# Kernel tuning notes

Hardware: AMD Instinct MI355X
Metric: run time of the kernel (lower is better)

Reference implementation:

```python
import jax, jax.numpy as jnp
import numpy as np

B, C, H, W = 8, 128, 48, 48
GROUPS = 32
EPS = 1e-5


def group_norm(x, w, b):
    # x: [B,C,H,W] -> normalize within 32 groups over (C//G, H, W)
    xg = x.reshape(B, GROUPS, C // GROUPS, H, W)
    mu = xg.mean(axis=(2, 3, 4), keepdims=True)
    var = xg.var(axis=(2, 3, 4), keepdims=True)
    xg = (xg - mu) * jax.lax.rsqrt(var + EPS)
    return xg.reshape(B, C, H, W) * w[None, :, None, None] + b[None, :, None, None]


def conv1x1(x, w, b):
    # pointwise conv: [B,C,H,W], w: [Cout,Cin], b: [Cout]
    return jnp.einsum('oc,bchw->bohw', w, x) + b[None, :, None, None]


def setup_inputs() -> dict:
    key = jax.random.key(0)
    ks = jax.random.split(key, 6)
    s = 1.0 / np.sqrt(C)
    return {
        'x': jax.random.normal(ks[0], (B, C, H, W), jnp.float32),
        'gn_w': jnp.ones((C,), jnp.float32),
        'gn_b': jnp.zeros((C,), jnp.float32),
        'wq': jax.random.normal(ks[1], (C, C), jnp.float32) * s,
        'bq': jnp.zeros((C,), jnp.float32),
        'wk': jax.random.normal(ks[2], (C, C), jnp.float32) * s,
        'bk': jnp.zeros((C,), jnp.float32),
        'wv': jax.random.normal(ks[3], (C, C), jnp.float32) * s,
        'bv': jnp.zeros((C,), jnp.float32),
        'wo': jax.random.normal(ks[4], (C, C), jnp.float32) * s,
        'bo': jnp.zeros((C,), jnp.float32),
    }


def reference(x, gn_w, gn_b, wq, bq, wk, bk, wv, bv, wo, bo):
    xn = group_norm(x, gn_w, gn_b)
    q = conv1x1(xn, wq, bq)
    k = conv1x1(xn, wk, bk)
    v = conv1x1(xn, wv, bv)
    # scores: [B,H,W,I,J]
    scores = jnp.einsum('bchw,bcij->bhwij', q, k) / jnp.sqrt(jnp.float32(C))
    # NOTE: original calls F.softmax with no dim; torch picks dim=1 (the query-H axis)
    attn = jax.nn.softmax(scores, axis=1)
    ctx = jnp.einsum('bhwnm,bcnm->bchw', attn, v)
    return x + conv1x1(ctx, wo, bo)
```

## Files before the change

kernel.cpp:

```cpp
#include <hip/hip_runtime.h>
#include <hip/hip_bf16.h>

typedef short s16x8 __attribute__((ext_vector_type(8)));
typedef float f32x4 __attribute__((ext_vector_type(4)));
typedef int   i32x4 __attribute__((ext_vector_type(4)));
typedef unsigned short u16;

#define BB 8
#define CC 128
#define HH 48
#define WW 48
#define NN 2304
#define SCALE_L2E 0.12751744f
#define SZ_MAP (BB*CC*NN)
#define NSPLIT 3
#define TILES_PER (18/NSPLIT)

__device__ inline u16 f2bf(float f) {
    unsigned u = __builtin_bit_cast(unsigned, f);
    u = (u + 0x7FFFu + ((u >> 16) & 1u)) >> 16;
    return (u16)u;
}
__device__ inline float bf2f(u16 h) {
    unsigned u = ((unsigned)h) << 16;
    return __builtin_bit_cast(float, u);
}

#define MFMA(a, b, c) __builtin_amdgcn_mfma_f32_16x16x32_bf16(a, b, c, 0, 0, 0)
#define DPP_ROR_ADD(x, N) { \
    int yi_ = __builtin_amdgcn_update_dpp(0, __builtin_bit_cast(int, x), 0x120 | (N), 0xf, 0xf, true); \
    x += __builtin_bit_cast(float, yi_); }

__global__ __launch_bounds__(256) void gnprep_kernel(
        const float* __restrict__ x, const float* __restrict__ gw,
        const float* __restrict__ gb, u16* __restrict__ xnT,
        const float* __restrict__ wq, const float* __restrict__ wk,
        const float* __restrict__ wv_, const float* __restrict__ wo,
        u16* __restrict__ w16) {
    int tid = threadIdx.x;
    if (blockIdx.x >= 256) {
        int i = (blockIdx.x - 256) * 256 + tid;
        int m = i >> 14, r = i & 16383;
        const float* src = (m == 0) ? wq : (m == 1) ? wk : (m == 2) ? wv_ : wo;
        w16[i] = f2bf(src[r]);
        return;
    }
    int b = blockIdx.x & 7, g = blockIdx.x >> 3;
    const float* xb = x + ((size_t)b * CC + g * 4) * NN;
    float v[4][9];
    float s = 0.f, ss = 0.f;
#pragma unroll
    for (int c = 0; c < 4; ++c)
#pragma unroll
        for (int k = 0; k < 9; ++k) {
            float t = xb[c * NN + tid + k * 256];
            v[c][k] = t; s += t; ss += t * t;
        }
#pragma unroll
    for (int o = 32; o > 0; o >>= 1) { s += __shfl_down(s, o); ss += __shfl_down(ss, o); }
    __shared__ float red[8];
    __shared__ float stats[2];
    int wid = tid >> 6;
    if ((tid & 63) == 0) { red[wid * 2] = s; red[wid * 2 + 1] = ss; }
    __syncthreads();
    if (tid == 0) {
        float S = 0.f, SS = 0.f;
        for (int i = 0; i < 4; ++i) { S += red[i * 2]; SS += red[i * 2 + 1]; }
        float mu = S * (1.f / 9216.f);
        float var = SS * (1.f / 9216.f) - mu * mu;
        stats[0] = mu;
        stats[1] = rsqrtf(var + 1e-5f);
    }
    __syncthreads();
    float mu = stats[0], rs = stats[1];
    float sc[4], bi[4];
#pragma unroll
    for (int c = 0; c < 4; ++c) {
        sc[c] = gw[g * 4 + c] * rs;
        bi[c] = gb[g * 4 + c] - mu * sc[c];
    }
#pragma unroll
    for (int k = 0; k < 9; ++k) {
        int n = tid + k * 256;
        ushort4 o;
        o.x = f2bf(v[0][k] * sc[0] + bi[0]);
        o.y = f2bf(v[1][k] * sc[1] + bi[1]);
        o.z = f2bf(v[2][k] * sc[2] + bi[2]);
        o.w = f2bf(v[3][k] * sc[3] + bi[3]);
        *(ushort4*)(xnT + ((size_t)b * NN + n) * CC + g * 4) = o;
    }
}

__global__ __launch_bounds__(256) void qkv_kernel(
        const u16* __restrict__ xnT, const u16* __restrict__ w16,
        const float* __restrict__ bq, const float* __restrict__ bk,
        const float* __restrict__ bv,
        u16* __restrict__ qT, u16* __restrict__ kt2, u16* __restrict__ vt2) {
    int b = blockIdx.x, n0 = blockIdx.y * 128, z = blockIdx.z;
    int tid = threadIdx.x, lane = tid & 63, wvw = tid >> 6;
    int l15 = lane & 15, l4 = lane >> 4;
    const u16* xb = xnT + (size_t)b * NN * CC;

    if (z == 0) {
        const u16* w16q = w16;
        const u16* w16k = w16 + 16384;
        u16* kb = kt2 + (size_t)b * NN * CC;
        s16x8 xa[2][4];
#pragma unroll
        for (int mf = 0; mf < 2; ++mf)
#pragma unroll
            for (int ks = 0; ks < 4; ++ks)
                xa[mf][ks] = *(const s16x8*)(xb + (size_t)(n0 + wvw * 32 + mf * 16 + l15) * CC + ks * 32 + l4 * 8);
        int chunk = blockIdx.y * 4 + wvw;
#pragma unroll 2
        for (int nf = 0; nf < 8; ++nf) {
            f32x4 aq[2] = {}, ak[2] = {};
#pragma unroll
            for (int ks = 0; ks < 4; ++ks) {
                s16x8 fq = *(const s16x8*)(w16q + (nf * 16 + l15) * CC + ks * 32 + l4 * 8);
                s16x8 fk = *(const s16x8*)(w16k + (nf * 16 + l15) * CC + ks * 32 + l4 * 8);
#pragma unroll
                for (int mf = 0; mf < 2; ++mf) {
                    aq[mf] = MFMA(fq, xa[mf][ks], aq[mf]);
                    ak[mf] = MFMA(fk, xa[mf][ks], ak[mf]);
                }
            }
            int cob = nf * 16 + l4 * 4;
            float4 bq4 = *(const float4*)(bq + cob);
            float4 bk4 = *(const float4*)(bk + cob);
#pragma unroll
            for (int mf = 0; mf < 2; ++mf) {
                int n = n0 + wvw * 32 + mf * 16 + l15;
                ushort4 qo;
                qo.x = f2bf((aq[mf][0] + bq4.x) * SCALE_L2E);
                qo.y = f2bf((aq[mf][1] + bq4.y) * SCALE_L2E);
                qo.z = f2bf((aq[mf][2] + bq4.z) * SCALE_L2E);
                qo.w = f2bf((aq[mf][3] + bq4.w) * SCALE_L2E);
                *(ushort4*)(qT + ((size_t)b * NN + n) * CC + cob) = qo;
                int n5 = mf * 16 + l15;
                int slot = ((n5 & 4) << 2) + ((n5 & 24) >> 1) + (n5 & 3);
                ushort4 ko;
                ko.x = f2bf(ak[mf][0] + bk4.x);
                ko.y = f2bf(ak[mf][1] + bk4.y);
                ko.z = f2bf(ak[mf][2] + bk4.z);
                ko.w = f2bf(ak[mf][3] + bk4.w);
                *(ushort4*)(kb + (size_t)chunk * 4096 + (cob >> 5) * 1024 + slot * 32 + (cob & 31)) = ko;
            }
        }
    } else {
        const u16* w16v = w16 + 2 * 16384;
        u16* vb = vt2 + (size_t)b * NN * CC;
        s16x8 wa[2][4];
#pragma unroll
        for (int mf = 0; mf < 2; ++mf)
#pragma unroll
            for (int ks = 0; ks < 4; ++ks)
                wa[mf][ks] = *(const s16x8*)(w16v + (wvw * 32 + mf * 16 + l15) * CC + ks * 32 + l4 * 8);
        float bvl[2];
        bvl[0] = bv[wvw * 32 + l15];
        bvl[1] = bv[wvw * 32 + 16 + l15];
#pragma unroll 2
        for (int nf = 0; nf < 8; ++nf) {
            f32x4 av[2] = {};
#pragma unroll
            for (int ks = 0; ks < 4; ++ks) {
                s16x8 xf = *(const s16x8*)(xb + (size_t)(n0 + nf * 16 + l15) * CC + ks * 32 + l4 * 8);
#pragma unroll
                for (int mf = 0; mf < 2; ++mf) av[mf] = MFMA(xf, wa[mf][ks], av[mf]);
            }
            int chunk = blockIdx.y * 4 + (nf >> 1);
            int nlo = (nf & 1) * 16 + l4 * 4;
#pragma unroll
            for (int mf = 0; mf < 2; ++mf) {
                ushort4 vo;
                vo.x = f2bf(av[mf][0] + bvl[mf]);
                vo.y = f2bf(av[mf][1] + bvl[mf]);
                vo.z = f2bf(av[mf][2] + bvl[mf]);
                vo.w = f2bf(av[mf][3] + bvl[mf]);
                *(ushort4*)(vb + (size_t)chunk * 4096 + (wvw * 2 + mf) * 512 + l15 * 32 + nlo) = vo;
            }
        }
    }
}

#define TILE_BODY(T, KFC, KFN) { \
    const u16* cv = vb + (size_t)((T) * 4 + wvw) * 4096; \
    s16x8 vf[8]; \
    _Pragma("unroll") \
    for (int cf = 0; cf < 8; ++cf) \
        vf[cf] = *(const s16x8*)(cv + cf * 512 + l15 * 32 + l4 * 8); \
    f32x4 sf[2][3] = {}; \
    __builtin_amdgcn_s_setprio(1); \
    _Pragma("unroll") \
    for (int ks = 0; ks < 4; ++ks) \
        _Pragma("unroll") \
        for (int mf = 0; mf < 2; ++mf) \
            _Pragma("unroll") \
            for (int hf = 0; hf < 3; ++hf) \
                sf[mf][hf] = MFMA(KFC[mf][ks], qf[hf][ks], sf[mf][hf]); \
    __builtin_amdgcn_s_setprio(0); \
    { \
        int tn_ = ((T) + 1 < 18) ? (T) + 1 : 0; \
        const u16* cbn_ = kb + (size_t)(tn_ * 4 + wvw) * 4096; \
        _Pragma("unroll") \
        for (int mf = 0; mf < 2; ++mf) \
            _Pragma("unroll") \
            for (int ks = 0; ks < 4; ++ks) \
                KFN[mf][ks] = *(const s16x8*)(cbn_ + ks * 1024 + (mf * 16 + l15) * 32 + l4 * 8); \
    } \
    float p[2][3][4]; \
    _Pragma("unroll") \
    for (int mf = 0; mf < 2; ++mf) \
        _Pragma("unroll") \
        for (int hf = 0; hf < 3; ++hf) \
            _Pragma("unroll") \
            for (int r = 0; r < 4; ++r) p[mf][hf][r] = __builtin_amdgcn_exp2f(sf[mf][hf][r]); \
    float den[2][4]; \
    _Pragma("unroll") \
    for (int mf = 0; mf < 2; ++mf) \
        _Pragma("unroll") \
        for (int r = 0; r < 4; ++r) \
            den[mf][r] = p[mf][0][r] + p[mf][1][r] + p[mf][2][r]; \
    _Pragma("unroll") \
    for (int mf = 0; mf < 2; ++mf) \
        _Pragma("unroll") \
        for (int r = 0; r < 4; ++r) { \
            DPP_ROR_ADD(den[mf][r], 1); \
            DPP_ROR_ADD(den[mf][r], 2); \
            DPP_ROR_ADD(den[mf][r], 4); \
            DPP_ROR_ADD(den[mf][r], 8); \
        } \
    float rd[2][4]; \
    _Pragma("unroll") \
    for (int mf = 0; mf < 2; ++mf) \
        _Pragma("unroll") \
        for (int r = 0; r < 4; ++r) rd[mf][r] = __builtin_amdgcn_rcpf(den[mf][r]); \
    s16x8 pbf[3]; \
    _Pragma("unroll") \
    for (int hf = 0; hf < 3; ++hf) { \
        unsigned u0, u1, u2, u3; \
        float a0 = p[0][hf][0] * rd[0][0], a1 = p[0][hf][1] * rd[0][1]; \
        float a2 = p[0][hf][2] * rd[0][2], a3 = p[0][hf][3] * rd[0][3]; \
        float a4 = p[1][hf][0] * rd[1][0], a5 = p[1][hf][1] * rd[1][1]; \
        float a6 = p[1][hf][2] * rd[1][2], a7 = p[1][hf][3] * rd[1][3]; \
        asm("v_cvt_pk_bf16_f32 %0, %1, %2" : "=v"(u0) : "v"(a0), "v"(a1)); \
        asm("v_cvt_pk_bf16_f32 %0, %1, %2" : "=v"(u1) : "v"(a2), "v"(a3)); \
        asm("v_cvt_pk_bf16_f32 %0, %1, %2" : "=v"(u2) : "v"(a4), "v"(a5)); \
        asm("v_cvt_pk_bf16_f32 %0, %1, %2" : "=v"(u3) : "v"(a6), "v"(a7)); \
        i32x4 bb2 = { (int)u0, (int)u1, (int)u2, (int)u3 }; \
        pbf[hf] = __builtin_bit_cast(s16x8, bb2); \
    } \
    __builtin_amdgcn_s_setprio(1); \
    _Pragma("unroll") \
    for (int cf = 0; cf < 8; ++cf) \
        _Pragma("unroll") \
        for (int hf = 0; hf < 3; ++hf) \
            cacc[cf][hf] = MFMA(vf[cf], pbf[hf], cacc[cf][hf]); \
    __builtin_amdgcn_s_setprio(0); \
}

__global__ __launch_bounds__(256, 2) void attn_kernel(
        const u16* __restrict__ qT, const u16* __restrict__ kt2,
        const u16* __restrict__ vt2, u16* __restrict__ part) {
    int b = blockIdx.x, w = blockIdx.y, sp = blockIdx.z;
    int tid = threadIdx.x, lane = tid & 63, wvw = tid >> 6;
    int l15 = lane & 15, l4 = lane >> 4;
    __shared__ float red[4 * 48 * 36];

    const u16* qb = qT + (size_t)b * NN * CC;
    const u16* kb = kt2 + (size_t)b * NN * CC;
    const u16* vb = vt2 + (size_t)b * NN * CC;

    s16x8 qf[3][4];
#pragma unroll
    for (int hf = 0; hf < 3; ++hf)
#pragma unroll
        for (int ks = 0; ks < 4; ++ks)
            qf[hf][ks] = *(const s16x8*)(qb + (size_t)((hf * 16 + l15) * WW + w) * CC + ks * 32 + l4 * 8);

    f32x4 cacc[8][3] = {};

    const int tbase = sp * TILES_PER;

    s16x8 kfA[2][4], kfB[2][4];
    {
        const u16* cb = kb + (size_t)(tbase * 4 + wvw) * 4096;
#pragma unroll
        for (int mf = 0; mf < 2; ++mf)
#pragma unroll
            for (int ks = 0; ks < 4; ++ks)
                kfA[mf][ks] = *(const s16x8*)(cb + ks * 1024 + (mf * 16 + l15) * 32 + l4 * 8);
    }

#pragma unroll 1
    for (int tt = 0; tt < TILES_PER; tt += 2) {
        int t0 = tbase + tt;
        TILE_BODY(t0, kfA, kfB)
        int t1 = tbase + tt + 1;
        TILE_BODY(t1, kfB, kfA)
    }

#pragma unroll
    for (int s = 0; s < 4; ++s) {
        if (s) __syncthreads();
#pragma unroll
        for (int q = 0; q < 4; ++q) {
            if (((q - wvw) & 3) == s) {
#pragma unroll
                for (int i = 0; i < 2; ++i) {
                    int cf = 2 * q + i;
#pragma unroll
                    for (int hf = 0; hf < 3; ++hf) {
                        int addr = q * 1728 + (hf * 16 + l15) * 36 + i * 16 + 4 * l4;
                        f32x4* pp = (f32x4*)&red[addr];
                        if (s == 0) *pp = cacc[cf][hf];
                        else { f32x4 tv = *pp; tv += cacc[cf][hf]; *pp = tv; }
                    }
                }
            }
        }
    }
    __syncthreads();
    u16* po = part + (size_t)(b * NSPLIT + sp) * NN * CC;
#pragma unroll
    for (int pass = 0; pass < 12; ++pass) {
        int h = pass * 4 + l4;
        int c = wvw * 32 + l15 * 2;
        float2 v2 = *(float2*)&red[wvw * 1728 + h * 36 + l15 * 2];
        unsigned pk;
        asm("v_cvt_pk_bf16_f32 %0, %1, %2" : "=v"(pk) : "v"(v2.x), "v"(v2.y));
        *(unsigned*)(po + (size_t)(h * WW + w) * CC + c) = pk;
    }
}

__global__ __launch_bounds__(256) void out_kernel(
        const u16* __restrict__ part, const u16* __restrict__ w16o,
        const float* __restrict__ bo, const float* __restrict__ x,
        float* __restrict__ out) {
    int b = blockIdx.x, n0 = blockIdx.y * 128;
    int tid = threadIdx.x, lane = tid & 63, wvw = tid >> 6;
    int l15 = lane & 15, l4 = lane >> 4;
    const u16* pb = part + (size_t)b * NSPLIT * NN * CC;
    s16x8 bfr[2][4];
#pragma unroll
    for (int nf = 0; nf < 2; ++nf)
#pragma unroll
        for (int ks = 0; ks < 4; ++ks) {
            size_t off = (size_t)(n0 + wvw * 32 + nf * 16 + l15) * CC + ks * 32 + l4 * 8;
            s16x8 v0 = *(const s16x8*)(pb + off);
            s16x8 v1 = *(const s16x8*)(pb + (size_t)NN * CC + off);
            s16x8 v2 = *(const s16x8*)(pb + (size_t)2 * NN * CC + off);
            s16x8 o;
#pragma unroll
            for (int j = 0; j < 8; ++j)
                o[j] = (short)f2bf(bf2f((u16)v0[j]) + bf2f((u16)v1[j]) + bf2f((u16)v2[j]));
            bfr[nf][ks] = o;
        }
#pragma unroll 2
    for (int mf = 0; mf < 8; ++mf) {
        s16x8 af[4];
#pragma unroll
        for (int ks = 0; ks < 4; ++ks)
            af[ks] = *(const s16x8*)(w16o + (mf * 16 + l15) * CC + ks * 32 + l4 * 8);
        f32x4 acc[2] = {};
#pragma unroll
        for (int ks = 0; ks < 4; ++ks)
#pragma unroll
            for (int nf = 0; nf < 2; ++nf)
                acc[nf] = MFMA(af[ks], bfr[nf][ks], acc[nf]);
#pragma unroll
        for (int nf = 0; nf < 2; ++nf)
#pragma unroll
            for (int r = 0; r < 4; ++r) {
                int co = mf * 16 + l4 * 4 + r;
                int n = n0 + wvw * 32 + nf * 16 + l15;
                size_t idx = ((size_t)b * CC + co) * NN + n;
                out[idx] = acc[nf][r] + bo[co] + x[idx];
            }
    }
}

extern "C" void kernel_launch(void* const* d_in, const int* in_sizes, int n_in,
                              void* d_out, int out_size, void* d_ws, size_t ws_size,
                              hipStream_t stream) {
    const float* x  = (const float*)d_in[0];
    const float* gw = (const float*)d_in[1];
    const float* gb = (const float*)d_in[2];
    const float* wq = (const float*)d_in[3];
    const float* bq = (const float*)d_in[4];
    const float* wk = (const float*)d_in[5];
    const float* bk = (const float*)d_in[6];
    const float* wv_ = (const float*)d_in[7];
    const float* bv = (const float*)d_in[8];
    const float* wo = (const float*)d_in[9];
    const float* bo = (const float*)d_in[10];

    u16* ws   = (u16*)d_ws;
    u16* xnT  = ws;
    u16* qT   = ws + (size_t)SZ_MAP;
    u16* kt2  = ws + (size_t)2 * SZ_MAP;
    u16* vt2  = ws + (size_t)3 * SZ_MAP;
    u16* part = ws + (size_t)4 * SZ_MAP;
    u16* w16  = ws + (size_t)(4 + NSPLIT) * SZ_MAP;
    float* out = (float*)d_out;

    gnprep_kernel<<<512, 256, 0, stream>>>(x, gw, gb, xnT, wq, wk, wv_, wo, w16);
    qkv_kernel<<<dim3(8, 18, 2), 256, 0, stream>>>(xnT, w16, bq, bk, bv, qT, kt2, vt2);
    attn_kernel<<<dim3(8, WW, NSPLIT), 256, 0, stream>>>(qT, kt2, vt2, part);
    out_kernel<<<dim3(8, 18), 256, 0, stream>>>(part, w16 + 3 * 16384, bo, x, out);
}
```

Baseline: 84.78 us.

## Restructure attention to share K/V chunks via LDS across eight w-waves

The attention kernel now assigns one w-column per wave (eight waves per 512-thread block). K/V chunks are staged into double-buffered LDS with global_load_lds and shared by all waves, which removes the old cross-wave LDS reduction. The goal is less redundant global K/V traffic. NSPLIT rises to 4. The QKV kernel splits Q and K into separate z-slices for more parallelism, and the output kernel splits output channels across two z-blocks and writes float4-vectorized output. The cost is a __syncthreads per chunk, an extra partial buffer to read and sum, and a higher register load from holding full cacc per wave.

New measurement: 77.59 us. 8.5% less time.

```diff
diff --git a/kernel.cpp b/kernel.cpp
--- a/kernel.cpp
+++ b/kernel.cpp
@@ -13,8 +13,8 @@
 #define NN 2304
 #define SCALE_L2E 0.12751744f
 #define SZ_MAP (BB*CC*NN)
-#define NSPLIT 3
-#define TILES_PER (18/NSPLIT)
+#define NSPLIT 4
+#define CHPER (72/NSPLIT)
 
 __device__ inline u16 f2bf(float f) {
     unsigned u = __builtin_bit_cast(unsigned, f);
@@ -103,31 +103,24 @@
 
     if (z == 0) {
         const u16* w16q = w16;
-        const u16* w16k = w16 + 16384;
-        u16* kb = kt2 + (size_t)b * NN * CC;
         s16x8 xa[2][4];
 #pragma unroll
         for (int mf = 0; mf < 2; ++mf)
 #pragma unroll
             for (int ks = 0; ks < 4; ++ks)
                 xa[mf][ks] = *(const s16x8*)(xb + (size_t)(n0 + wvw * 32 + mf * 16 + l15) * CC + ks * 32 + l4 * 8);
-        int chunk = blockIdx.y * 4 + wvw;
 #pragma unroll 2
         for (int nf = 0; nf < 8; ++nf) {
-            f32x4 aq[2] = {}, ak[2] = {};
+            f32x4 aq[2] = {};
 #pragma unroll
             for (int ks = 0; ks < 4; ++ks) {
                 s16x8 fq = *(const s16x8*)(w16q + (nf * 16 + l15) * CC + ks * 32 + l4 * 8);
-                s16x8 fk = *(const s16x8*)(w16k + (nf * 16 + l15) * CC + ks * 32 + l4 * 8);
-#pragma unroll
-                for (int mf = 0; mf < 2; ++mf) {
+#pragma unroll
+                for (int mf = 0; mf < 2; ++mf)
                     aq[mf] = MFMA(fq, xa[mf][ks], aq[mf]);
-                    ak[mf] = MFMA(fk, xa[mf][ks], ak[mf]);
-                }
             }
             int cob = nf * 16 + l4 * 4;
             float4 bq4 = *(const float4*)(bq + cob);
-            float4 bk4 = *(const float4*)(bk + cob);
 #pragma unroll
             for (int mf = 0; mf < 2; ++mf) {
                 int n = n0 + wvw * 32 + mf * 16 + l15;
@@ -137,6 +130,32 @@
                 qo.z = f2bf((aq[mf][2] + bq4.z) * SCALE_L2E);
                 qo.w = f2bf((aq[mf][3] + bq4.w) * SCALE_L2E);
                 *(ushort4*)(qT + ((size_t)b * NN + n) * CC + cob) = qo;
+            }
+        }
+    } else if (z == 1) {
+        const u16* w16k = w16 + 16384;
+        u16* kb = kt2 + (size_t)b * NN * CC;
+        s16x8 xa[2][4];
+#pragma unroll
+        for (int mf = 0; mf < 2; ++mf)
+#pragma unroll
+            for (int ks = 0; ks < 4; ++ks)
+                xa[mf][ks] = *(const s16x8*)(xb + (size_t)(n0 + wvw * 32 + mf * 16 + l15) * CC + ks * 32 + l4 * 8);
+        int chunk = blockIdx.y * 4 + wvw;
+#pragma unroll 2
+        for (int nf = 0; nf < 8; ++nf) {
+            f32x4 ak[2] = {};
+#pragma unroll
+            for (int ks = 0; ks < 4; ++ks) {
+                s16x8 fk = *(const s16x8*)(w16k + (nf * 16 + l15) * CC + ks * 32 + l4 * 8);
+#pragma unroll
+                for (int mf = 0; mf < 2; ++mf)
+                    ak[mf] = MFMA(fk, xa[mf][ks], ak[mf]);
+            }
+            int cob = nf * 16 + l4 * 4;
+            float4 bk4 = *(const float4*)(bk + cob);
+#pragma unroll
+            for (int mf = 0; mf < 2; ++mf) {
                 int n5 = mf * 16 + l15;
                 int slot = ((n5 & 4) << 2) + ((n5 & 24) >> 1) + (n5 & 3);
                 ushort4 ko;
@@ -183,44 +202,43 @@
     }
 }
 
-#define TILE_BODY(T, KFC, KFN) { \
-    const u16* cv = vb + (size_t)((T) * 4 + wvw) * 4096; \
-    s16x8 vf[8]; \
-    _Pragma("unroll") \
-    for (int cf = 0; cf < 8; ++cf) \
-        vf[cf] = *(const s16x8*)(cv + cf * 512 + l15 * 32 + l4 * 8); \
+#define STAGE(CH, KD, VD) { \
+    const u16* ks_ = kb + (size_t)(CH) * 4096 + wvw * 512 + lane * 8; \
+    const u16* vs_ = vb + (size_t)(CH) * 4096 + wvw * 512 + lane * 8; \
+    __builtin_amdgcn_global_load_lds((const __attribute__((address_space(1))) void*)ks_, \
+        (__attribute__((address_space(3))) void*)(KD + wvw * 512), 16, 0, 0); \
+    __builtin_amdgcn_global_load_lds((const __attribute__((address_space(1))) void*)vs_, \
+        (__attribute__((address_space(3))) void*)(VD + wvw * 512), 16, 0, 0); \
+}
+
+#define CHUNK_BODY(CH, KC, VC, KN, VN) { \
+    { int nx_ = ((CH) + 1 < 72) ? (CH) + 1 : 0; STAGE(nx_, KN, VN) } \
     f32x4 sf[2][3] = {}; \
     __builtin_amdgcn_s_setprio(1); \
     _Pragma("unroll") \
-    for (int ks = 0; ks < 4; ++ks) \
-        _Pragma("unroll") \
-        for (int mf = 0; mf < 2; ++mf) \
-            _Pragma("unroll") \
-            for (int hf = 0; hf < 3; ++hf) \
-                sf[mf][hf] = MFMA(KFC[mf][ks], qf[hf][ks], sf[mf][hf]); \
+    for (int ks = 0; ks < 4; ++ks) { \
+        s16x8 kf0 = *(const s16x8*)(KC + ks * 1024 + l15 * 32 + l4 * 8); \
+        s16x8 kf1 = *(const s16x8*)(KC + ks * 1024 + (16 + l15) * 32 + l4 * 8); \
+        _Pragma("unroll") \
+        for (int hf = 0; hf < 3; ++hf) { \
+            sf[0][hf] = MFMA(kf0, qf[hf][ks], sf[0][hf]); \
+            sf[1][hf] = MFMA(kf1, qf[hf][ks], sf[1][hf]); \
+        } \
+    } \
     __builtin_amdgcn_s_setprio(0); \
-    { \
-        int tn_ = ((T) + 1 < 18) ? (T) + 1 : 0; \
-        const u16* cbn_ = kb + (size_t)(tn_ * 4 + wvw) * 4096; \
-        _Pragma("unroll") \
-        for (int mf = 0; mf < 2; ++mf) \
-            _Pragma("unroll") \
-            for (int ks = 0; ks < 4; ++ks) \
-                KFN[mf][ks] = *(const s16x8*)(cbn_ + ks * 1024 + (mf * 16 + l15) * 32 + l4 * 8); \
-    } \
-    float p[2][3][4]; \
+    float pe[2][3][4]; \
     _Pragma("unroll") \
     for (int mf = 0; mf < 2; ++mf) \
         _Pragma("unroll") \
         for (int hf = 0; hf < 3; ++hf) \
             _Pragma("unroll") \
-            for (int r = 0; r < 4; ++r) p[mf][hf][r] = __builtin_amdgcn_exp2f(sf[mf][hf][r]); \
+            for (int r = 0; r < 4; ++r) pe[mf][hf][r] = __builtin_amdgcn_exp2f(sf[mf][hf][r]); \
     float den[2][4]; \
     _Pragma("unroll") \
     for (int mf = 0; mf < 2; ++mf) \
         _Pragma("unroll") \
         for (int r = 0; r < 4; ++r) \
-            den[mf][r] = p[mf][0][r] + p[mf][1][r] + p[mf][2][r]; \
+            den[mf][r] = pe[mf][0][r] + pe[mf][1][r] + pe[mf][2][r]; \
     _Pragma("unroll") \
     for (int mf = 0; mf < 2; ++mf) \
         _Pragma("unroll") \
@@ -239,10 +257,10 @@
     _Pragma("unroll") \
     for (int hf = 0; hf < 3; ++hf) { \
         unsigned u0, u1, u2, u3; \
-        float a0 = p[0][hf][0] * rd[0][0], a1 = p[0][hf][1] * rd[0][1]; \
-        float a2 = p[0][hf][2] * rd[0][2], a3 = p[0][hf][3] * rd[0][3]; \
-        float a4 = p[1][hf][0] * rd[1][0], a5 = p[1][hf][1] * rd[1][1]; \
-        float a6 = p[1][hf][2] * rd[1][2], a7 = p[1][hf][3] * rd[1][3]; \
+        float a0 = pe[0][hf][0] * rd[0][0], a1 = pe[0][hf][1] * rd[0][1]; \
+        float a2 = pe[0][hf][2] * rd[0][2], a3 = pe[0][hf][3] * rd[0][3]; \
+        float a4 = pe[1][hf][0] * rd[1][0], a5 = pe[1][hf][1] * rd[1][1]; \
+        float a6 = pe[1][hf][2] * rd[1][2], a7 = pe[1][hf][3] * rd[1][3]; \
         asm("v_cvt_pk_bf16_f32 %0, %1, %2" : "=v"(u0) : "v"(a0), "v"(a1)); \
         asm("v_cvt_pk_bf16_f32 %0, %1, %2" : "=v"(u1) : "v"(a2), "v"(a3)); \
         asm("v_cvt_pk_bf16_f32 %0, %1, %2" : "=v"(u2) : "v"(a4), "v"(a5)); \
@@ -252,20 +270,24 @@
     } \
     __builtin_amdgcn_s_setprio(1); \
     _Pragma("unroll") \
-    for (int cf = 0; cf < 8; ++cf) \
+    for (int cf = 0; cf < 8; ++cf) { \
+        s16x8 vf = *(const s16x8*)(VC + cf * 512 + l15 * 32 + l4 * 8); \
         _Pragma("unroll") \
         for (int hf = 0; hf < 3; ++hf) \
-            cacc[cf][hf] = MFMA(vf[cf], pbf[hf], cacc[cf][hf]); \
+            cacc[cf][hf] = MFMA(vf, pbf[hf], cacc[cf][hf]); \
+    } \
     __builtin_amdgcn_s_setprio(0); \
-}
-
-__global__ __launch_bounds__(256, 2) void attn_kernel(
+    __syncthreads(); \
+}
+
+__global__ __launch_bounds__(512, 2) void attn_kernel(
         const u16* __restrict__ qT, const u16* __restrict__ kt2,
         const u16* __restrict__ vt2, u16* __restrict__ part) {
-    int b = blockIdx.x, w = blockIdx.y, sp = blockIdx.z;
+    int b = blockIdx.x, sp = blockIdx.z;
     int tid = threadIdx.x, lane = tid & 63, wvw = tid >> 6;
+    int w = blockIdx.y * 8 + wvw;
     int l15 = lane & 15, l4 = lane >> 4;
-    __shared__ float red[4 * 48 * 36];
+    __shared__ u16 kbA[4096], vbA[4096], kbB[4096], vbB[4096];
 
     const u16* qb = qT + (size_t)b * NN * CC;
     const u16* kb = kt2 + (size_t)b * NN * CC;
@@ -280,64 +302,38 @@
 
     f32x4 cacc[8][3] = {};
 
-    const int tbase = sp * TILES_PER;
-
-    s16x8 kfA[2][4], kfB[2][4];
-    {
-        const u16* cb = kb + (size_t)(tbase * 4 + wvw) * 4096;
-#pragma unroll
-        for (int mf = 0; mf < 2; ++mf)
-#pragma unroll
-            for (int ks = 0; ks < 4; ++ks)
-                kfA[mf][ks] = *(const s16x8*)(cb + ks * 1024 + (mf * 16 + l15) * 32 + l4 * 8);
-    }
+    const int cbase = sp * CHPER;
+    STAGE(cbase, kbA, vbA)
+    __syncthreads();
 
 #pragma unroll 1
-    for (int tt = 0; tt < TILES_PER; tt += 2) {
-        int t0 = tbase + tt;
-        TILE_BODY(t0, kfA, kfB)
-        int t1 = tbase + tt + 1;
-        TILE_BODY(t1, kfB, kfA)
-    }
-
-#pragma unroll
-    for (int s = 0; s < 4; ++s) {
-        if (s) __syncthreads();
-#pragma unroll
-        for (int q = 0; q < 4; ++q) {
-            if (((q - wvw) & 3) == s) {
-#pragma unroll
-                for (int i = 0; i < 2; ++i) {
-                    int cf = 2 * q + i;
-#pragma unroll
-                    for (int hf = 0; hf < 3; ++hf) {
-                        int addr = q * 1728 + (hf * 16 + l15) * 36 + i * 16 + 4 * l4;
-                        f32x4* pp = (f32x4*)&red[addr];
-                        if (s == 0) *pp = cacc[cf][hf];
-                        else { f32x4 tv = *pp; tv += cacc[cf][hf]; *pp = tv; }
-                    }
-                }
-            }
-        }
-    }
-    __syncthreads();
+    for (int ii = 0; ii < CHPER; ii += 2) {
+        int c0 = cbase + ii;
+        CHUNK_BODY(c0, kbA, vbA, kbB, vbB)
+        int c1 = cbase + ii + 1;
+        CHUNK_BODY(c1, kbB, vbB, kbA, vbA)
+    }
+
     u16* po = part + (size_t)(b * NSPLIT + sp) * NN * CC;
 #pragma unroll
-    for (int pass = 0; pass < 12; ++pass) {
-        int h = pass * 4 + l4;
-        int c = wvw * 32 + l15 * 2;
-        float2 v2 = *(float2*)&red[wvw * 1728 + h * 36 + l15 * 2];
-        unsigned pk;
-        asm("v_cvt_pk_bf16_f32 %0, %1, %2" : "=v"(pk) : "v"(v2.x), "v"(v2.y));
-        *(unsigned*)(po + (size_t)(h * WW + w) * CC + c) = pk;
-    }
+    for (int cf = 0; cf < 8; ++cf)
+#pragma unroll
+        for (int hf = 0; hf < 3; ++hf) {
+            int h = hf * 16 + l15;
+            int c0 = cf * 16 + l4 * 4;
+            unsigned pk01, pk23;
+            asm("v_cvt_pk_bf16_f32 %0, %1, %2" : "=v"(pk01) : "v"(cacc[cf][hf][0]), "v"(cacc[cf][hf][1]));
+            asm("v_cvt_pk_bf16_f32 %0, %1, %2" : "=v"(pk23) : "v"(cacc[cf][hf][2]), "v"(cacc[cf][hf][3]));
+            uint2 pk = { pk01, pk23 };
+            *(uint2*)(po + (size_t)(h * WW + w) * CC + c0) = pk;
+        }
 }
 
 __global__ __launch_bounds__(256) void out_kernel(
         const u16* __restrict__ part, const u16* __restrict__ w16o,
         const float* __restrict__ bo, const float* __restrict__ x,
         float* __restrict__ out) {
-    int b = blockIdx.x, n0 = blockIdx.y * 128;
+    int b = blockIdx.x, n0 = blockIdx.y * 128, zh = blockIdx.z;
     int tid = threadIdx.x, lane = tid & 63, wvw = tid >> 6;
     int l15 = lane & 15, l4 = lane >> 4;
     const u16* pb = part + (size_t)b * NSPLIT * NN * CC;
@@ -350,14 +346,17 @@
             s16x8 v0 = *(const s16x8*)(pb + off);
             s16x8 v1 = *(const s16x8*)(pb + (size_t)NN * CC + off);
             s16x8 v2 = *(const s16x8*)(pb + (size_t)2 * NN * CC + off);
+            s16x8 v3 = *(const s16x8*)(pb + (size_t)3 * NN * CC + off);
             s16x8 o;
 #pragma unroll
             for (int j = 0; j < 8; ++j)
-                o[j] = (short)f2bf(bf2f((u16)v0[j]) + bf2f((u16)v1[j]) + bf2f((u16)v2[j]));
+                o[j] = (short)f2bf(bf2f((u16)v0[j]) + bf2f((u16)v1[j])
+                                   + bf2f((u16)v2[j]) + bf2f((u16)v3[j]));
             bfr[nf][ks] = o;
         }
-#pragma unroll 2
-    for (int mf = 0; mf < 8; ++mf) {
+#pragma unroll
+    for (int mi = 0; mi < 4; ++mi) {
+        int mf = zh * 4 + mi;
         s16x8 af[4];
 #pragma unroll
         for (int ks = 0; ks < 4; ++ks)
@@ -367,16 +366,21 @@
         for (int ks = 0; ks < 4; ++ks)
 #pragma unroll
             for (int nf = 0; nf < 2; ++nf)
-                acc[nf] = MFMA(af[ks], bfr[nf][ks], acc[nf]);
-#pragma unroll
-        for (int nf = 0; nf < 2; ++nf)
-#pragma unroll
-            for (int r = 0; r < 4; ++r) {
-                int co = mf * 16 + l4 * 4 + r;
-                int n = n0 + wvw * 32 + nf * 16 + l15;
-                size_t idx = ((size_t)b * CC + co) * NN + n;
-                out[idx] = acc[nf][r] + bo[co] + x[idx];
-            }
+                acc[nf] = MFMA(bfr[nf][ks], af[ks], acc[nf]);
+        int co = mf * 16 + l15;
+        float bol = bo[co];
+#pragma unroll
+        for (int nf = 0; nf < 2; ++nf) {
+            int n = n0 + wvw * 32 + nf * 16 + l4 * 4;
+            size_t idx = ((size_t)b * CC + co) * NN + n;
+            float4 xr = *(const float4*)(x + idx);
+            float4 o4;
+            o4.x = acc[nf][0] + bol + xr.x;
+            o4.y = acc[nf][1] + bol + xr.y;
+            o4.z = acc[nf][2] + bol + xr.z;
+            o4.w = acc[nf][3] + bol + xr.w;
+            *(float4*)(out + idx) = o4;
+        }
     }
 }
 
@@ -405,7 +409,7 @@
     float* out = (float*)d_out;
 
     gnprep_kernel<<<512, 256, 0, stream>>>(x, gw, gb, xnT, wq, wk, wv_, wo, w16);
-    qkv_kernel<<<dim3(8, 18, 2), 256, 0, stream>>>(xnT, w16, bq, bk, bv, qT, kt2, vt2);
-    attn_kernel<<<dim3(8, WW, NSPLIT), 256, 0, stream>>>(qT, kt2, vt2, part);
-    out_kernel<<<dim3(8, 18), 256, 0, stream>>>(part, w16 + 3 * 16384, bo, x, out);
-}
+    qkv_kernel<<<dim3(8, 18, 3), 256, 0, stream>>>(xnT, w16, bq, bk, bv, qT, kt2, vt2);
+    attn_kernel<<<dim3(8, 6, NSPLIT), 512, 0, stream>>>(qT, kt2, vt2, part);
+    out_kernel<<<dim3(8, 18, 2), 256, 0, stream>>>(part, w16 + 3 * 16384, bo, x, out);
+}
```
